# Performance work log

Measured on AMD Instinct MI355X. Metric: run time of the kernel, lower is better.

## Reference

```python
import jax, jax.numpy as jnp
import numpy as np

B, I, H, O, K = 256, 512, 512, 512, 256


def setup_inputs() -> dict:
    key = jax.random.key(0)
    ks = jax.random.split(key, 16)
    def lin(kw, kb, out_dim, in_dim):
        s = 1.0 / np.sqrt(in_dim)
        W = jax.random.uniform(kw, (out_dim, in_dim), jnp.float32, -s, s)
        b = jax.random.uniform(kb, (out_dim,), jnp.float32, -s, s)
        return W, b
    Wd, bd = lin(ks[0], ks[1], H, I + 2 * H)
    Wr, br = lin(ks[2], ks[3], H, I + H)
    Wz, bz = lin(ks[4], ks[5], H, I + H)
    Wh, bh = lin(ks[6], ks[7], H, I + H)
    Wo, bo = lin(ks[8], ks[9], O, H)
    return {
        "sample": jax.random.normal(ks[10], (B, I), jnp.float32),
        "hidden": jax.random.normal(ks[11], (B, H), jnp.float32),
        "hidden_tensor": jax.random.normal(ks[12], (K, B, H), jnp.float32),
        "d_0": jax.random.normal(ks[13], (B, H), jnp.float32),
        "Wd": Wd, "bd": bd, "Wr": Wr, "br": br,
        "Wz": Wz, "bz": bz, "Wh": Wh, "bh": bh, "Wo": Wo, "bo": bo,
    }


def _filter_d(hidden_tensor, d_values):
    # get_ws: w[j] = prod_{m=0}^{K-1-j} (m - d) / (m + 1)  for j in [0, K)
    # Vectorized: cumprod of (m-d)/(m+1) along m, then flip.
    m = jnp.arange(K, dtype=d_values.dtype).reshape(K, 1, 1)  # [K,1,1]
    factors = (m - d_values[None, :, :]) / (m + 1.0)          # [K,B,H]
    w = jnp.flip(jnp.cumprod(factors, axis=0), axis=0)        # [K,B,H]
    return jnp.sum(hidden_tensor * w, axis=0)                 # [B,H]


def reference(sample, hidden, hidden_tensor, d_0,
              Wd, bd, Wr, br, Wz, bz, Wh, bh, Wo, bo):
    combined = jnp.concatenate([sample, hidden], axis=1)          # [B, I+H]
    combined_d = jnp.concatenate([sample, hidden, d_0], axis=1)   # [B, I+2H]

    d_values = jax.nn.sigmoid(combined_d @ Wd.T + bd) * 0.5       # [B,H]
    first = -_filter_d(hidden_tensor, d_values)                   # [B,H]

    r_gate = jax.nn.sigmoid(combined @ Wr.T + br)
    z_gate = jax.nn.sigmoid(combined @ Wz.T + bz)

    combined2 = jnp.concatenate([sample, r_gate * hidden], axis=1)
    h_tilde = jnp.tanh(combined2 @ Wh.T + bh)
    second = h_tilde * (1.0 - z_gate)

    hidden_new = first + second                                   # [B,H]
    h_c_1 = jnp.concatenate([hidden_tensor, hidden_new[None]], axis=0)[1:]  # [K,B,H]
    output = hidden_new @ Wo.T + bo                               # [B,O]
    return (output, hidden_new, h_c_1, d_values)
```

## Files before the change

kernel.cpp:

```cpp
#include <hip/hip_runtime.h>
#include <cstddef>

#define B_ 256
#define H_ 512
#define KF 256
#define BH 131072
#define BH2 65536
#define BH4 32768
#define H4 128

#define BM 64
#define BN 64
#define BK 16

typedef float nf4 __attribute__((ext_vector_type(4)));

__device__ __forceinline__ float sigmoidf_(float x) { return 1.0f / (1.0f + __expf(-x)); }
__device__ __forceinline__ float tanh_fast(float x) { return 2.0f / (1.0f + __expf(-2.0f * x)) - 1.0f; }
__device__ __forceinline__ float4 sig4(float4 v) {
    return make_float4(sigmoidf_(v.x), sigmoidf_(v.y), sigmoidf_(v.z), sigmoidf_(v.w));
}

#define MAC_LOOP()                                                         \
    _Pragma("unroll")                                                      \
    for (int kk = 0; kk < BK; ++kk) {                                      \
        const float4 a = *(const float4*)&As[kk][ty << 2];                 \
        const float4 w = *(const float4*)&Ws[kk][tx << 2];                 \
        const float a4[4] = {a.x, a.y, a.z, a.w};                          \
        const float w4[4] = {w.x, w.y, w.z, w.w};                          \
        _Pragma("unroll")                                                  \
        for (int i = 0; i < 4; ++i)                                        \
            _Pragma("unroll")                                              \
            for (int j = 0; j < 4; ++j)                                    \
                acc[i][j] = fmaf(a4[i], w4[j], acc[i][j]);                 \
    }

template<bool MUL>
__device__ __forceinline__ void gemm64(
    float (*As)[BM + 4], float (*Ws)[BN + 4],
    const float* __restrict__ abase, const float* __restrict__ rbase,
    const float* __restrict__ W, int Ktot, int ks,
    int bm, int bn, int nIter, float* __restrict__ p)
{
    const int tid = threadIdx.x;
    const int ty = tid >> 4, tx = tid & 15;
    const int lrow = tid >> 2, lcol = (tid & 3) << 2;
    const float* aptr = abase + (bm + lrow) * 512 + lcol;
    const float* rptr = MUL ? rbase + (bm + lrow) * 512 + lcol : nullptr;
    const float* wptr = W + (size_t)(bn + lrow) * Ktot + ks + lcol;

    float acc[4][4] = {};
    float4 av = *(const float4*)aptr;
    if (MUL) { const float4 rv = *(const float4*)rptr;
               av.x *= rv.x; av.y *= rv.y; av.z *= rv.z; av.w *= rv.w; }
    float4 wv = *(const float4*)wptr;

    for (int it = 0; it < nIter; ++it) {
        __syncthreads();
        As[lcol + 0][lrow] = av.x; As[lcol + 1][lrow] = av.y;
        As[lcol + 2][lrow] = av.z; As[lcol + 3][lrow] = av.w;
        Ws[lcol + 0][lrow] = wv.x; Ws[lcol + 1][lrow] = wv.y;
        Ws[lcol + 2][lrow] = wv.z; Ws[lcol + 3][lrow] = wv.w;
        __syncthreads();
        if (it < nIter - 1) {
            av = *(const float4*)(aptr + (it + 1) * BK);
            if (MUL) { const float4 rv = *(const float4*)(rptr + (it + 1) * BK);
                       av.x *= rv.x; av.y *= rv.y; av.z *= rv.z; av.w *= rv.w; }
            wv = *(const float4*)(wptr + (it + 1) * BK);
        }
        MAC_LOOP();
    }
    #pragma unroll
    for (int i = 0; i < 4; ++i) {
        const int m = bm + (ty << 2) + i;
        #pragma unroll
        for (int j = 0; j < 4; ++j)
            p[m * 512 + bn + (tx << 2) + j] = acc[i][j];
    }
}

__global__ __launch_bounds__(256) void k_gemm_drz(
    const float* __restrict__ sample, const float* __restrict__ hidden,
    const float* __restrict__ d0,
    const float* __restrict__ Wd, const float* __restrict__ Wr,
    const float* __restrict__ Wz,
    float* __restrict__ dbase, float* __restrict__ rzbase)
{
    __shared__ float As[BK][BM + 4];
    __shared__ float Ws[BK][BN + 4];
    const int z = blockIdx.z;
    if (z < 6) {
        const int ks = z << 8, seg = ks >> 9;
        const float* ab = (seg == 0 ? sample : (seg == 1 ? hidden : d0)) + (ks & 511);
        gemm64<false>(As, Ws, ab, nullptr, Wd, 1536, ks,
                      blockIdx.y * BM, blockIdx.x * BN, 16, dbase + (size_t)z * BH);
    } else {
        const int id = z - 6, gz = id >> 2, s = id & 3, ks = s << 8;
        const float* ab = (ks < 512 ? sample + ks : hidden + (ks - 512));
        gemm64<false>(As, Ws, ab, nullptr, gz ? Wz : Wr, 1024, ks,
                      blockIdx.y * BM, blockIdx.x * BN, 16, rzbase + (size_t)id * BH);
    }
}

__global__ __launch_bounds__(256) void k_dv(
    const float4* __restrict__ dparts, const float4* __restrict__ bd,
    const float4* __restrict__ rzparts, const float4* __restrict__ br,
    const float4* __restrict__ bz,
    float4* __restrict__ dv4, float4* __restrict__ rb4, float4* __restrict__ zb4)
{
    const int g = blockIdx.x * 256 + threadIdx.x;
    const int n = g & (H4 - 1);
    float4 sd = bd[n], sr = br[n], sz = bz[n];
    #pragma unroll
    for (int s = 0; s < 6; ++s) { const float4 p = dparts[(size_t)s * BH4 + g];
        sd.x += p.x; sd.y += p.y; sd.z += p.z; sd.w += p.w; }
    #pragma unroll
    for (int s = 0; s < 4; ++s) { const float4 p = rzparts[(size_t)s * BH4 + g];
        sr.x += p.x; sr.y += p.y; sr.z += p.z; sr.w += p.w; }
    #pragma unroll
    for (int s = 4; s < 8; ++s) { const float4 p = rzparts[(size_t)s * BH4 + g];
        sz.x += p.x; sz.y += p.y; sz.z += p.z; sz.w += p.w; }
    const float4 d = sig4(sd);
    dv4[g] = make_float4(0.5f * d.x, 0.5f * d.y, 0.5f * d.z, 0.5f * d.w);
    rb4[g] = sig4(sr);
    zb4[g] = sig4(sz);
}

#define FLOADB(buf, b)                                                     \
    _Pragma("unroll")                                                      \
    for (int u = 0; u < 8; ++u)                                            \
        buf[u] = ld_base[-(ptrdiff_t)((b) * 8 + u) * BH4];

#define FCSTORE(buf, b)                                                    \
    _Pragma("unroll")                                                      \
    for (int u = 0; u < 8; ++u) {                                          \
        const int t = t0 + (b) * 8 + u;                                    \
        const float iv = s_inv[t], tv = s_tinv[t];                         \
        c.x *= fmaf(-d.x, iv, tv); c.y *= fmaf(-d.y, iv, tv);              \
        c.z *= fmaf(-d.z, iv, tv); c.w *= fmaf(-d.w, iv, tv);              \
        a.x = fmaf(buf[u].x, c.x, a.x); a.y = fmaf(buf[u].y, c.y, a.y);    \
        a.z = fmaf(buf[u].z, c.z, a.z); a.w = fmaf(buf[u].w, c.w, a.w);    \
        __builtin_nontemporal_store(*(const nf4*)&buf[u],                  \
            (nf4*)(st_base - (ptrdiff_t)((b) * 8 + u) * BH4));             \
    }

__global__ __launch_bounds__(256, 4) void k_mega(
    const float4* __restrict__ ht4, const float4* __restrict__ dv4,
    const float* __restrict__ sample, const float* __restrict__ hidden,
    const float* __restrict__ rb, const float* __restrict__ Wh,
    float* __restrict__ ws, float4* __restrict__ hc14)
{
    if (blockIdx.x < 128) {
        __shared__ float As[BK][BM + 4];
        __shared__ float Wsh[BK][BN + 4];
        const int id = blockIdx.x;
        const int s = id >> 5, t2 = id & 31;
        const int bn = (t2 >> 2) << 6, bm = (t2 & 3) << 6, ks = s << 8;
        if (ks < 512)
            gemm64<false>(As, Wsh, sample + ks, nullptr, Wh, 1024, ks, bm, bn, 16,
                          ws + (size_t)s * BH);
        else
            gemm64<true>(As, Wsh, hidden + (ks - 512), rb + (ks - 512), Wh, 1024, ks,
                         bm, bn, 16, ws + (size_t)s * BH);
        return;
    }
    __shared__ float s_inv[KF], s_tinv[KF];
    const int tid = threadIdx.x;
    const float fi = 1.0f / (float)(tid + 1);
    s_inv[tid] = fi; s_tinv[tid] = (float)tid * fi;
    __syncthreads();

    const int fb  = blockIdx.x - 128;
    const int seg = fb >> 7;
    const int q   = ((fb & 127) << 8) | tid;
    const float4 d = dv4[q];
    const int t0 = seg << 5;

    const float4* ld_base = ht4 + (size_t)(255 - t0) * BH4 + q;
    float4*       st_base = hc14 + (ptrdiff_t)(254 - t0) * BH4 + q;

    float4 c = make_float4(1.f, 1.f, 1.f, 1.f);
    float4 a = make_float4(0.f, 0.f, 0.f, 0.f);

    float4 va[8], vb[8];
    FLOADB(va, 0);
    FLOADB(vb, 1);
    FCSTORE(va, 0);
    FLOADB(va, 2);
    FCSTORE(vb, 1);
    FLOADB(vb, 3);
    FCSTORE(va, 2);
    FCSTORE(vb, 3);

    const int slice = (seg < 4) ? (4 + seg) : (6 + seg);
    ((float4*)ws)[(size_t)slice * BH4 + q] = a;
}

__global__ __launch_bounds__(256) void k_finalize(
    const float4* __restrict__ dv4, const float4* __restrict__ ws4,
    const float4* __restrict__ bh, const float4* __restrict__ zb4,
    float4* hc1_4, float4* __restrict__ hn_out)
{
    __shared__ float s_inv[224], s_tinv[224];
    const int tid = threadIdx.x;
    if (tid < 224) { const float fi = 1.0f / (float)(tid + 1);
                     s_inv[tid] = fi; s_tinv[tid] = (float)tid * fi; }
    __syncthreads();

    const int g = blockIdx.x * 256 + tid;
    const int n = g & (H4 - 1);
    const float4 d = dv4[g];

    float4 acc = ws4[(size_t)4 * BH4 + g];
    float4 c = make_float4(1.f, 1.f, 1.f, 1.f);
    #pragma unroll
    for (int sgm = 1; sgm < 8; ++sgm) {
        #pragma unroll
        for (int t = (sgm - 1) * 32; t < sgm * 32; ++t) {
            const float iv = s_inv[t], tv = s_tinv[t];
            c.x *= fmaf(-d.x, iv, tv); c.y *= fmaf(-d.y, iv, tv);
            c.z *= fmaf(-d.z, iv, tv); c.w *= fmaf(-d.w, iv, tv);
        }
        const int sl = (sgm < 4) ? (4 + sgm) : (6 + sgm);
        const float4 ai = ws4[(size_t)sl * BH4 + g];
        acc.x = fmaf(c.x, ai.x, acc.x); acc.y = fmaf(c.y, ai.y, acc.y);
        acc.z = fmaf(c.z, ai.z, acc.z); acc.w = fmaf(c.w, ai.w, acc.w);
    }

    float4 hs = bh[n];
    #pragma unroll
    for (int s = 0; s < 4; ++s) { const float4 p = ws4[(size_t)s * BH4 + g];
        hs.x += p.x; hs.y += p.y; hs.z += p.z; hs.w += p.w; }
    const float4 z = zb4[g];

    float4 hn;
    hn.x = tanh_fast(hs.x) * (1.0f - z.x) - acc.x;
    hn.y = tanh_fast(hs.y) * (1.0f - z.y) - acc.y;
    hn.z = tanh_fast(hs.z) * (1.0f - z.z) - acc.z;
    hn.w = tanh_fast(hs.w) * (1.0f - z.w) - acc.w;
    hn_out[g] = hn;
    hc1_4[(size_t)255 * BH4 + g] = hn;
}

__global__ __launch_bounds__(256) void k_gemm_o(
    const float* __restrict__ hn, const float* __restrict__ Wo,
    float* __restrict__ parts, int chunk)
{
    __shared__ float As[BK][BM + 4];
    __shared__ float Ws[BK][BN + 4];
    const int s = blockIdx.z, ks = s * chunk;
    gemm64<false>(As, Ws, hn + ks, nullptr, Wo, 512, ks,
                  blockIdx.y * BM, blockIdx.x * BN, chunk / BK, parts + (size_t)s * BH);
}

__global__ __launch_bounds__(256) void k_reduce_o(
    const float4* parts, const float4* __restrict__ bo, float4* out, int NS)
{
    const int g = blockIdx.x * 256 + threadIdx.x;
    float4 v = bo[g & (H4 - 1)];
    for (int s = 0; s < NS; ++s) { const float4 p = parts[(size_t)s * BH4 + g];
        v.x += p.x; v.y += p.y; v.z += p.z; v.w += p.w; }
    out[g] = v;
}

__global__ __launch_bounds__(256) void k_reduce_rz(
    const float4* __restrict__ parts, const float4* __restrict__ br,
    const float4* __restrict__ bz, float4* __restrict__ rb, float4* __restrict__ zb)
{
    const int g = blockIdx.x * 256 + threadIdx.x;
    const int n = g & (H4 - 1);
    float4 r = br[n], z = bz[n];
    #pragma unroll
    for (int s = 0; s < 4; ++s) { const float4 p = parts[(size_t)s * BH4 + g];
        r.x += p.x; r.y += p.y; r.z += p.z; r.w += p.w; }
    #pragma unroll
    for (int s = 4; s < 8; ++s) { const float4 p = parts[(size_t)s * BH4 + g];
        z.x += p.x; z.y += p.y; z.z += p.z; z.w += p.w; }
    rb[g] = sig4(r); zb[g] = sig4(z);
}

__global__ __launch_bounds__(256) void k_gemm_h(
    const float* __restrict__ sample, const float* __restrict__ hidden,
    const float* __restrict__ rb, const float* __restrict__ Wh,
    float* __restrict__ parts)
{
    __shared__ float As[BK][BM + 4];
    __shared__ float Ws[BK][BN + 4];
    const int s = blockIdx.z, ks = s << 8;
    if (ks < 512)
        gemm64<false>(As, Ws, sample + ks, nullptr, Wh, 1024, ks,
                      blockIdx.y * BM, blockIdx.x * BN, 16, parts + (size_t)s * BH);
    else
        gemm64<true>(As, Ws, hidden + (ks - 512), rb + (ks - 512), Wh, 1024, ks,
                     blockIdx.y * BM, blockIdx.x * BN, 16, parts + (size_t)s * BH);
}

__global__ __launch_bounds__(256) void k_filter_full(
    const float* __restrict__ ht, const float* dparts, const float* __restrict__ bd,
    const float* zbuf, const float* hparts, const float* __restrict__ bh,
    float* hc1, float* __restrict__ dv_out, float* __restrict__ hn_out)
{
    __shared__ float s_inv[KF], s_tinv[KF];
    const int tid = threadIdx.x;
    const float fi = 1.0f / (float)(tid + 1);
    s_inv[tid] = fi; s_tinv[tid] = (float)tid * fi;
    __syncthreads();

    const int g = blockIdx.x * 256 + tid;
    const int n = g & (H_ - 1);
    float sd = bd[n];
    #pragma unroll
    for (int s = 0; s < 6; ++s) sd += dparts[(size_t)s * BH + g];
    const float d = 0.5f * sigmoidf_(sd);
    dv_out[g] = d;
    float sh = bh[n];
    #pragma unroll
    for (int s = 0; s < 4; ++s) sh += hparts[(size_t)s * BH + g];
    const float z = zbuf[g];

    float c = 1.0f, acc = 0.0f;
    #pragma unroll 16
    for (int t = 0; t < KF; ++t) {
        const int k = KF - 1 - t;
        const float v = ht[(size_t)k * BH + g];
        c *= fmaf(-d, s_inv[t], s_tinv[t]);
        acc = fmaf(v, c, acc);
        if (k >= 1) hc1[(size_t)(k - 1) * BH + g] = v;
    }
    const float hn = tanh_fast(sh) * (1.0f - z) - acc;
    hc1[(size_t)(KF - 1) * BH + g] = hn;
    hn_out[g] = hn;
}

extern "C" void kernel_launch(void* const* d_in, const int* in_sizes, int n_in,
                              void* d_out, int out_size, void* d_ws, size_t ws_size,
                              hipStream_t stream)
{
    const float* sample = (const float*)d_in[0];
    const float* hidden = (const float*)d_in[1];
    const float* ht     = (const float*)d_in[2];
    const float* d0     = (const float*)d_in[3];
    const float* Wd = (const float*)d_in[4];
    const float* bd = (const float*)d_in[5];
    const float* Wr = (const float*)d_in[6];
    const float* br = (const float*)d_in[7];
    const float* Wz = (const float*)d_in[8];
    const float* bz = (const float*)d_in[9];
    const float* Wh = (const float*)d_in[10];
    const float* bh = (const float*)d_in[11];
    const float* Wo = (const float*)d_in[12];
    const float* bo = (const float*)d_in[13];

    float* out     = (float*)d_out;
    float* out_o   = out;
    float* out_hn  = out + BH;
    float* out_hc1 = out + 2 * BH;
    float* out_dv  = out + 2 * BH + (size_t)KF * BH;

    const size_t slice = BH;
    const size_t need = 14ull * slice * sizeof(float);

    if (ws_size >= need) {
        float* ws = (float*)d_ws;
        float* rb = ws + 8 * slice;
        float* zb = ws + 9 * slice;

        k_gemm_drz<<<dim3(8, 4, 14), 256, 0, stream>>>(sample, hidden, d0,
                                                       Wd, Wr, Wz, out_hc1, ws);
        k_dv<<<dim3(128), 256, 0, stream>>>(
            (const float4*)out_hc1, (const float4*)bd,
            (const float4*)ws, (const float4*)br, (const float4*)bz,
            (float4*)out_dv, (float4*)rb, (float4*)zb);
        k_mega<<<dim3(1152), 256, 0, stream>>>(
            (const float4*)ht, (const float4*)out_dv, sample, hidden, rb, Wh,
            ws, (float4*)out_hc1);
        k_finalize<<<dim3(128), 256, 0, stream>>>(
            (const float4*)out_dv, (const float4*)ws,
            (const float4*)bh, (const float4*)zb,
            (float4*)out_hc1, (float4*)out_hn);
        k_gemm_o<<<dim3(8, 4, 4), 256, 0, stream>>>(out_hn, Wo, ws, 128);
        k_reduce_o<<<dim3(128), 256, 0, stream>>>((const float4*)ws,
                                                  (const float4*)bo,
                                                  (float4*)out_o, 4);
    } else {
        float* sl = out_hc1;
        k_gemm_drz<<<dim3(8, 4, 14), 256, 0, stream>>>(sample, hidden, d0,
                                                       Wd, Wr, Wz, sl, sl + 6 * slice);
        k_reduce_rz<<<dim3(128), 256, 0, stream>>>((const float4*)(sl + 6 * slice),
                                                   (const float4*)br, (const float4*)bz,
                                                   (float4*)(sl + 14 * slice),
                                                   (float4*)(sl + 15 * slice));
        k_gemm_h<<<dim3(8, 4, 4), 256, 0, stream>>>(sample, hidden, sl + 14 * slice, Wh,
                                                    sl + 16 * slice);
        k_filter_full<<<dim3(512), 256, 0, stream>>>(ht, sl, bd, sl + 15 * slice,
                                                     sl + 16 * slice, bh,
                                                     out_hc1, out_dv, out_hn);
        k_gemm_o<<<dim3(8, 4, 1), 256, 0, stream>>>(out_hn, Wo, out_o, 512);
        k_reduce_o<<<dim3(128), 256, 0, stream>>>((const float4*)out_o, (const float4*)bo,
                                                  (float4*)out_o, 1);
    }
}
```

Baseline: 84.96 us.

## Interleave filter time steps across segments so finalize needs no cumprod chain

The fractional filter previously gave each of 8 segment blocks a contiguous run of 32 time steps, and k_finalize then rebuilt the cumulative-product scaling chain for every segment. Now segment `seg` handles time steps seg, seg+8, seg+16 and so on. Each thread computes its own coefficient prefix up to seg and then advances the product by 8 factors per step. This makes every segment's partial sum already fully scaled, so k_finalize only adds 8 slices and no longer needs the d_values read or the serial 224-step product chain. In exchange the filter blocks do roughly 8x more multiply-FMA work per step, and each block's loads are strided by 8 time slices instead of being contiguous.

```diff
diff --git a/kernel.cpp b/kernel.cpp
--- a/kernel.cpp
+++ b/kernel.cpp
@@ -5,7 +5,6 @@
 #define H_ 512
 #define KF 256
 #define BH 131072
-#define BH2 65536
 #define BH4 32768
 #define H4 128
 
@@ -129,19 +128,26 @@
 #define FLOADB(buf, b)                                                     \
     _Pragma("unroll")                                                      \
     for (int u = 0; u < 8; ++u)                                            \
-        buf[u] = ld_base[-(ptrdiff_t)((b) * 8 + u) * BH4];
+        buf[u] = ld_base[-(ptrdiff_t)(8 * ((b) * 8 + u)) * BH4];
 
 #define FCSTORE(buf, b)                                                    \
     _Pragma("unroll")                                                      \
     for (int u = 0; u < 8; ++u) {                                          \
-        const int t = t0 + (b) * 8 + u;                                    \
-        const float iv = s_inv[t], tv = s_tinv[t];                         \
-        c.x *= fmaf(-d.x, iv, tv); c.y *= fmaf(-d.y, iv, tv);              \
-        c.z *= fmaf(-d.z, iv, tv); c.w *= fmaf(-d.w, iv, tv);              \
+        const int j = (b) * 8 + u;                                         \
+        if (j > 0) {                                                       \
+            _Pragma("unroll")                                              \
+            for (int m = 0; m < 8; ++m) {                                  \
+                const float2 f = pf[8 * j - 7 + m];                        \
+                c.x *= fmaf(-d.x, f.x, f.y);                               \
+                c.y *= fmaf(-d.y, f.x, f.y);                               \
+                c.z *= fmaf(-d.z, f.x, f.y);                               \
+                c.w *= fmaf(-d.w, f.x, f.y);                               \
+            }                                                              \
+        }                                                                  \
         a.x = fmaf(buf[u].x, c.x, a.x); a.y = fmaf(buf[u].y, c.y, a.y);    \
         a.z = fmaf(buf[u].z, c.z, a.z); a.w = fmaf(buf[u].w, c.w, a.w);    \
         __builtin_nontemporal_store(*(const nf4*)&buf[u],                  \
-            (nf4*)(st_base - (ptrdiff_t)((b) * 8 + u) * BH4));             \
+            (nf4*)(st_base - (ptrdiff_t)(8 * j) * BH4));                   \
     }
 
 __global__ __launch_bounds__(256, 4) void k_mega(
@@ -164,22 +170,29 @@
                          bm, bn, 16, ws + (size_t)s * BH);
         return;
     }
-    __shared__ float s_inv[KF], s_tinv[KF];
+    __shared__ float2 s_f[KF];
     const int tid = threadIdx.x;
-    const float fi = 1.0f / (float)(tid + 1);
-    s_inv[tid] = fi; s_tinv[tid] = (float)tid * fi;
+    {
+        const float fi = 1.0f / (float)(tid + 1);
+        s_f[tid] = make_float2(fi, (float)tid * fi);
+    }
     __syncthreads();
 
     const int fb  = blockIdx.x - 128;
     const int seg = fb >> 7;
     const int q   = ((fb & 127) << 8) | tid;
     const float4 d = dv4[q];
-    const int t0 = seg << 5;
-
-    const float4* ld_base = ht4 + (size_t)(255 - t0) * BH4 + q;
-    float4*       st_base = hc14 + (ptrdiff_t)(254 - t0) * BH4 + q;
+
+    const float4* ld_base = ht4 + (size_t)(255 - seg) * BH4 + q;
+    float4*       st_base = hc14 + (ptrdiff_t)(254 - seg) * BH4 + q;
+    const float2* pf = &s_f[seg];
 
     float4 c = make_float4(1.f, 1.f, 1.f, 1.f);
+    for (int t = 0; t <= seg; ++t) {
+        const float2 f = s_f[t];
+        c.x *= fmaf(-d.x, f.x, f.y); c.y *= fmaf(-d.y, f.x, f.y);
+        c.z *= fmaf(-d.z, f.x, f.y); c.w *= fmaf(-d.w, f.x, f.y);
+    }
     float4 a = make_float4(0.f, 0.f, 0.f, 0.f);
 
     float4 va[8], vb[8];
@@ -197,36 +210,20 @@
 }
 
 __global__ __launch_bounds__(256) void k_finalize(
-    const float4* __restrict__ dv4, const float4* __restrict__ ws4,
-    const float4* __restrict__ bh, const float4* __restrict__ zb4,
+    const float4* __restrict__ ws4, const float4* __restrict__ bh,
+    const float4* __restrict__ zb4,
     float4* hc1_4, float4* __restrict__ hn_out)
 {
-    __shared__ float s_inv[224], s_tinv[224];
-    const int tid = threadIdx.x;
-    if (tid < 224) { const float fi = 1.0f / (float)(tid + 1);
-                     s_inv[tid] = fi; s_tinv[tid] = (float)tid * fi; }
-    __syncthreads();
-
-    const int g = blockIdx.x * 256 + tid;
+    const int g = blockIdx.x * 256 + threadIdx.x;
     const int n = g & (H4 - 1);
-    const float4 d = dv4[g];
-
-    float4 acc = ws4[(size_t)4 * BH4 + g];
-    float4 c = make_float4(1.f, 1.f, 1.f, 1.f);
-    #pragma unroll
-    for (int sgm = 1; sgm < 8; ++sgm) {
-        #pragma unroll
-        for (int t = (sgm - 1) * 32; t < sgm * 32; ++t) {
-            const float iv = s_inv[t], tv = s_tinv[t];
-            c.x *= fmaf(-d.x, iv, tv); c.y *= fmaf(-d.y, iv, tv);
-            c.z *= fmaf(-d.z, iv, tv); c.w *= fmaf(-d.w, iv, tv);
-        }
-        const int sl = (sgm < 4) ? (4 + sgm) : (6 + sgm);
+
+    float4 acc = make_float4(0.f, 0.f, 0.f, 0.f);
+    #pragma unroll
+    for (int s = 0; s < 8; ++s) {
+        const int sl = (s < 4) ? (4 + s) : (6 + s);
         const float4 ai = ws4[(size_t)sl * BH4 + g];
-        acc.x = fmaf(c.x, ai.x, acc.x); acc.y = fmaf(c.y, ai.y, acc.y);
-        acc.z = fmaf(c.z, ai.z, acc.z); acc.w = fmaf(c.w, ai.w, acc.w);
-    }
-
+        acc.x += ai.x; acc.y += ai.y; acc.z += ai.z; acc.w += ai.w;
+    }
     float4 hs = bh[n];
     #pragma unroll
     for (int s = 0; s < 4; ++s) { const float4 p = ws4[(size_t)s * BH4 + g];
@@ -375,8 +372,7 @@
             (const float4*)ht, (const float4*)out_dv, sample, hidden, rb, Wh,
             ws, (float4*)out_hc1);
         k_finalize<<<dim3(128), 256, 0, stream>>>(
-            (const float4*)out_dv, (const float4*)ws,
-            (const float4*)bh, (const float4*)zb,
+            (const float4*)ws, (const float4*)bh, (const float4*)zb,
             (float4*)out_hc1, (float4*)out_hn);
         k_gemm_o<<<dim3(8, 4, 4), 256, 0, stream>>>(out_hn, Wo, ws, 128);
         k_reduce_o<<<dim3(128), 256, 0, stream>>>((const float4*)ws,
```

Measured after the change: 116.8 us. +37.5%, slower.

## Split hidden_tensor shift-copy into dedicated copy blocks interleaved with filter blocks

Applied to the files above, without the earlier changes.

The filter blocks in the fused kernel no longer write the shifted hidden_tensor slices into h_c_1. Dedicated copy blocks now do that work with contiguous 8-float4-per-thread nontemporal copies, scheduled one filter block per four copy blocks, and the grid grows to match. The aim is to decouple the streaming copy from the strided filter accumulation and balance load and store traffic across the grid. In exchange, hidden_tensor is read twice, once by the filter blocks and once by the copy blocks, which adds substantial memory traffic unless the second read hits the cache.

```diff
diff --git a/kernel.cpp b/kernel.cpp
--- a/kernel.cpp
+++ b/kernel.cpp
@@ -5,7 +5,6 @@
 #define H_ 512
 #define KF 256
 #define BH 131072
-#define BH2 65536
 #define BH4 32768
 #define H4 128
 
@@ -131,7 +130,7 @@
     for (int u = 0; u < 8; ++u)                                            \
         buf[u] = ld_base[-(ptrdiff_t)((b) * 8 + u) * BH4];
 
-#define FCSTORE(buf, b)                                                    \
+#define FCACC(buf, b)                                                      \
     _Pragma("unroll")                                                      \
     for (int u = 0; u < 8; ++u) {                                          \
         const int t = t0 + (b) * 8 + u;                                    \
@@ -140,8 +139,6 @@
         c.z *= fmaf(-d.z, iv, tv); c.w *= fmaf(-d.w, iv, tv);              \
         a.x = fmaf(buf[u].x, c.x, a.x); a.y = fmaf(buf[u].y, c.y, a.y);    \
         a.z = fmaf(buf[u].z, c.z, a.z); a.w = fmaf(buf[u].w, c.w, a.w);    \
-        __builtin_nontemporal_store(*(const nf4*)&buf[u],                  \
-            (nf4*)(st_base - (ptrdiff_t)((b) * 8 + u) * BH4));             \
     }
 
 __global__ __launch_bounds__(256, 4) void k_mega(
@@ -150,11 +147,12 @@
     const float* __restrict__ rb, const float* __restrict__ Wh,
     float* __restrict__ ws, float4* __restrict__ hc14)
 {
-    if (blockIdx.x < 128) {
+    const int bid = blockIdx.x;
+    const int tid = threadIdx.x;
+    if (bid < 128) {
         __shared__ float As[BK][BM + 4];
         __shared__ float Wsh[BK][BN + 4];
-        const int id = blockIdx.x;
-        const int s = id >> 5, t2 = id & 31;
+        const int s = bid >> 5, t2 = bid & 31;
         const int bn = (t2 >> 2) << 6, bm = (t2 & 3) << 6, ks = s << 8;
         if (ks < 512)
             gemm64<false>(As, Wsh, sample + ks, nullptr, Wh, 1024, ks, bm, bn, 16,
@@ -164,20 +162,43 @@
                          bm, bn, 16, ws + (size_t)s * BH);
         return;
     }
+
+    const int id = bid - 128;
+    int fidx, cidx = -1;
+    if (id < 5100) {
+        const int grp = id / 5, slot = id - grp * 5;
+        if (slot == 0) fidx = grp;
+        else           cidx = grp * 4 + slot - 1;
+    } else {
+        fidx = 1020 + (id - 5100);
+    }
+
+    if (cidx >= 0) {
+        const size_t base = (size_t)cidx * 2048 + tid;
+        const float4* src = ht4 + BH4 + base;
+        float4* dst = hc14 + base;
+        float4 v[8];
+        #pragma unroll
+        for (int u = 0; u < 8; ++u) v[u] = src[(size_t)u * 256];
+        #pragma unroll
+        for (int u = 0; u < 8; ++u)
+            __builtin_nontemporal_store(*(const nf4*)&v[u], (nf4*)(dst + (size_t)u * 256));
+        return;
+    }
+
     __shared__ float s_inv[KF], s_tinv[KF];
-    const int tid = threadIdx.x;
-    const float fi = 1.0f / (float)(tid + 1);
-    s_inv[tid] = fi; s_tinv[tid] = (float)tid * fi;
+    {
+        const float fi = 1.0f / (float)(tid + 1);
+        s_inv[tid] = fi; s_tinv[tid] = (float)tid * fi;
+    }
     __syncthreads();
 
-    const int fb  = blockIdx.x - 128;
-    const int seg = fb >> 7;
-    const int q   = ((fb & 127) << 8) | tid;
+    const int seg = fidx >> 7;
+    const int q   = ((fidx & 127) << 8) | tid;
     const float4 d = dv4[q];
     const int t0 = seg << 5;
 
     const float4* ld_base = ht4 + (size_t)(255 - t0) * BH4 + q;
-    float4*       st_base = hc14 + (ptrdiff_t)(254 - t0) * BH4 + q;
 
     float4 c = make_float4(1.f, 1.f, 1.f, 1.f);
     float4 a = make_float4(0.f, 0.f, 0.f, 0.f);
@@ -185,12 +206,12 @@
     float4 va[8], vb[8];
     FLOADB(va, 0);
     FLOADB(vb, 1);
-    FCSTORE(va, 0);
+    FCACC(va, 0);
     FLOADB(va, 2);
-    FCSTORE(vb, 1);
+    FCACC(vb, 1);
     FLOADB(vb, 3);
-    FCSTORE(va, 2);
-    FCSTORE(vb, 3);
+    FCACC(va, 2);
+    FCACC(vb, 3);
 
     const int slice = (seg < 4) ? (4 + seg) : (6 + seg);
     ((float4*)ws)[(size_t)slice * BH4 + q] = a;
@@ -371,7 +392,7 @@
             (const float4*)out_hc1, (const float4*)bd,
             (const float4*)ws, (const float4*)br, (const float4*)bz,
             (float4*)out_dv, (float4*)rb, (float4*)zb);
-        k_mega<<<dim3(1152), 256, 0, stream>>>(
+        k_mega<<<dim3(5232), 256, 0, stream>>>(
             (const float4*)ht, (const float4*)out_dv, sample, hidden, rb, Wh,
             ws, (float4*)out_hc1);
         k_finalize<<<dim3(128), 256, 0, stream>>>(
```

Result: slower. 105.6 us (+24.3%).
